# Optimization experiments

Measured on AMD Instinct MI355X. Metric: run time of the kernel, lower is better.

Reference implementation:

```python
import jax, jax.numpy as jnp
import numpy as np

B, T, F, H = 64, 512, 128, 512

def _rnn(x_seq, h0, Wih, Whh, bih, bhh):
    # PyTorch vanilla RNN: h_t = tanh(x_t @ Wih^T + bih + h_{t-1} @ Whh^T + bhh)
    def step(h, x_t):
        h = jnp.tanh(x_t @ Wih.T + bih + h @ Whh.T + bhh)
        return h, h
    _, ys = jax.lax.scan(step, h0, jnp.swapaxes(x_seq, 0, 1))  # scan over time
    return jnp.swapaxes(ys, 0, 1)  # [B, T, H]

def _decode(z, Wih, Whh, bih, bhh):
    # decoder input at step t = concat(prev_output, z_t); 1-layer RNN so prev_output == h_{t-1}
    def step(h, z_t):
        u = jnp.concatenate([h, z_t], axis=-1)  # [B, 2H]
        h_new = jnp.tanh(u @ Wih.T + bih + h @ Whh.T + bhh)
        return h_new, h_new
    h0 = jnp.zeros((z.shape[0], Whh.shape[0]), z.dtype)
    _, ys = jax.lax.scan(step, h0, jnp.swapaxes(z, 0, 1))
    return jnp.swapaxes(ys, 0, 1)  # [B, T, H]

def setup_inputs() -> dict:
    key = jax.random.key(0)
    ks = jax.random.split(key, 16)
    s = 0.02
    p = {
        'x':   jax.random.normal(ks[0], (B, T, F), jnp.float32),
        'eps': jax.random.normal(ks[1], (B, T, H), jnp.float32),
        'Wih_en': jax.random.normal(ks[2], (H, F)) * s,
        'Whh_en': jax.random.normal(ks[3], (H, H)) * s,
        'bih_en': jax.random.normal(ks[4], (H,)) * s,
        'bhh_en': jax.random.normal(ks[5], (H,)) * s,
        'W_mu':  jax.random.normal(ks[6], (H, H)) * s,
        'b_mu':  jax.random.normal(ks[7], (H,)) * s,
        'W_lv':  jax.random.normal(ks[8], (H, H)) * s,
        'b_lv':  jax.random.normal(ks[9], (H,)) * s,
        'Wih_de': jax.random.normal(ks[10], (H, 2 * H)) * s,
        'Whh_de': jax.random.normal(ks[11], (H, H)) * s,
        'bih_de': jax.random.normal(ks[12], (H,)) * s,
        'bhh_de': jax.random.normal(ks[13], (H,)) * s,
        'W_mux': jax.random.normal(ks[14], (F, H)) * s,
        'b_mux': jnp.zeros((F,)),
        'W_lvx': jax.random.normal(ks[15], (F, H)) * s,
        'b_lvx': jnp.zeros((F,)),
    }
    return p

def reference(x, eps, Wih_en, Whh_en, bih_en, bhh_en, W_mu, b_mu, W_lv, b_lv,
              Wih_de, Whh_de, bih_de, bhh_de, W_mux, b_mux, W_lvx, b_lvx):
    h0 = jnp.zeros((x.shape[0], Whh_en.shape[0]), x.dtype)
    y = _rnn(x, h0, Wih_en, Whh_en, bih_en, bhh_en)                 # [B,T,H]
    mu_post = y @ W_mu.T + b_mu
    logsigma2_post = y @ W_lv.T + b_lv
    z = eps * jnp.exp(logsigma2_post / 2) + mu_post                 # reparameterize
    outputs = _decode(z, Wih_de, Whh_de, bih_de, bhh_de)            # [B,T,H]
    mu_xhat = outputs @ W_mux.T + b_mux
    logsigma2_xhat = outputs @ W_lvx.T + b_lvx
    return (mu_post, logsigma2_post, mu_xhat, logsigma2_xhat)
```

## Files before the change

kernel.cpp:

```cpp
#include <hip/hip_runtime.h>

typedef _Float16 h2_t __attribute__((ext_vector_type(2)));
typedef _Float16 h4_t __attribute__((ext_vector_type(4)));
typedef _Float16 h8_t __attribute__((ext_vector_type(8)));
typedef float    f4_t __attribute__((ext_vector_type(4)));

#define B_  64
#define T_  512
#define F_  128
#define H_  512

static __device__ __forceinline__ float fdot2f(h2_t a, h2_t b, float c) {
#if __has_builtin(__builtin_amdgcn_fdot2)
    return __builtin_amdgcn_fdot2(a, b, c, false);
#else
    return c + (float)a.x * (float)b.x + (float)a.y * (float)b.y;
#endif
}

static __device__ __forceinline__ void dot8(float& acc, uint4 w, uint4 h) {
    acc = fdot2f(__builtin_bit_cast(h2_t, w.x), __builtin_bit_cast(h2_t, h.x), acc);
    acc = fdot2f(__builtin_bit_cast(h2_t, w.y), __builtin_bit_cast(h2_t, h.y), acc);
    acc = fdot2f(__builtin_bit_cast(h2_t, w.z), __builtin_bit_cast(h2_t, h.z), acc);
    acc = fdot2f(__builtin_bit_cast(h2_t, w.w), __builtin_bit_cast(h2_t, h.w), acc);
}

static __device__ __forceinline__ int d4(int acc, unsigned a, unsigned b) {
#if __has_builtin(__builtin_amdgcn_sdot4)
    return __builtin_amdgcn_sdot4((int)a, (int)b, acc, false);
#else
    #pragma unroll
    for (int i = 0; i < 4; ++i)
        acc += (int)(signed char)((a >> (8 * i)) & 0xff) *
               (int)(signed char)((b >> (8 * i)) & 0xff);
    return acc;
#endif
}
static __device__ __forceinline__ int dot16i8(int acc, uint4 w, uint4 h) {
    acc = d4(acc, w.x, h.x);
    acc = d4(acc, w.y, h.y);
    acc = d4(acc, w.z, h.z);
    acc = d4(acc, w.w, h.w);
    return acc;
}

__global__ void k_cast_f16(const float* __restrict__ src, _Float16* __restrict__ dst, int n) {
    int i = blockIdx.x * blockDim.x + threadIdx.x;
    if (i < n) dst[i] = (_Float16)src[i];
}

__global__ void k_prep_z(const float* __restrict__ Wih_de, _Float16* __restrict__ Wz) {
    int i = blockIdx.x * blockDim.x + threadIdx.x;
    int cc = i >> 9, kk = i & 511;
    Wz[i] = (_Float16)Wih_de[cc * 1024 + 512 + kk];
}

__global__ void k_prep_bias(const float* __restrict__ a, const float* __restrict__ b,
                            float* __restrict__ o) {
    int i = threadIdx.x;
    o[i] = a[i] + b[i];
}

__global__ void k_quant(const float* __restrict__ A, int sA,
                        const float* __restrict__ Bo, int sB,
                        signed char* __restrict__ q, float* __restrict__ fac) {
    __shared__ float red[128];
    const int c = blockIdx.x, t = threadIdx.x;
    f4_t v = *(const f4_t*)(A + (size_t)c * sA + t * 4);
    if (Bo) {
        f4_t vb = *(const f4_t*)(Bo + (size_t)c * sB + t * 4);
        v = v + vb;
    }
    float m = fmaxf(fmaxf(fabsf(v[0]), fabsf(v[1])), fmaxf(fabsf(v[2]), fabsf(v[3])));
    red[t] = m;
    __syncthreads();
    for (int o = 64; o; o >>= 1) {
        if (t < o) red[t] = fmaxf(red[t], red[t + o]);
        __syncthreads();
    }
    float mx = red[0];
    float inv = mx > 0.f ? 127.f / mx : 0.f;
    unsigned r = 0;
    #pragma unroll
    for (int i = 0; i < 4; ++i) {
        int qi = (int)rintf(fminf(fmaxf(v[i] * inv, -127.f), 127.f));
        r |= ((unsigned)(unsigned char)(signed char)qi) << (8 * i);
    }
    *(unsigned*)(q + (size_t)c * 512 + t * 4) = r;
    if (t == 0) fac[c] = mx > 0.f ? mx / 127.f : 0.f;
}

#define BM 128
#define BN 128
#define BK 32
#define LDT 40

__global__ __launch_bounds__(256) void k_gemm(
    const _Float16* __restrict__ A, const _Float16* __restrict__ Bt,
    const float* __restrict__ bias,
    float* __restrict__ Cf, _Float16* __restrict__ Ch,
    int M, int N, int K) {
    __shared__ _Float16 Al[BM * LDT];
    __shared__ _Float16 Bl[BN * LDT];
    const int tid = threadIdx.x;
    const int bm = blockIdx.x * BM, bn = blockIdx.y * BN;
    const int wid = tid >> 6, lane = tid & 63;
    const int wm = (wid >> 1) * 64, wn = (wid & 1) * 64;
    const int l15 = lane & 15, l4 = lane >> 4;

    f4_t acc[4][4];
    #pragma unroll
    for (int i = 0; i < 4; ++i)
        #pragma unroll
        for (int j = 0; j < 4; ++j) {
            f4_t zz = {0.f, 0.f, 0.f, 0.f};
            acc[i][j] = zz;
        }

    const int r = tid >> 1, hf = tid & 1;
    const h8_t* gA0 = (const h8_t*)(A + (size_t)(bm + r) * K);
    const h8_t* gB0 = (const h8_t*)(Bt + (size_t)(bn + r) * K);

    for (int k0 = 0; k0 < K; k0 += BK) {
        __syncthreads();
        int kf = (k0 >> 3) + hf * 2;
        h8_t a0 = gA0[kf], a1 = gA0[kf + 1];
        h8_t b0 = gB0[kf], b1 = gB0[kf + 1];
        *(h8_t*)&Al[r * LDT + hf * 16]     = a0;
        *(h8_t*)&Al[r * LDT + hf * 16 + 8] = a1;
        *(h8_t*)&Bl[r * LDT + hf * 16]     = b0;
        *(h8_t*)&Bl[r * LDT + hf * 16 + 8] = b1;
        __syncthreads();
        h8_t af[4], bf[4];
        #pragma unroll
        for (int i = 0; i < 4; ++i) af[i] = *(const h8_t*)&Al[(wm + i * 16 + l15) * LDT + l4 * 8];
        #pragma unroll
        for (int j = 0; j < 4; ++j) bf[j] = *(const h8_t*)&Bl[(wn + j * 16 + l15) * LDT + l4 * 8];
        #pragma unroll
        for (int i = 0; i < 4; ++i)
            #pragma unroll
            for (int j = 0; j < 4; ++j)
                acc[i][j] = __builtin_amdgcn_mfma_f32_16x16x32_f16(af[i], bf[j], acc[i][j], 0, 0, 0);
    }

    #pragma unroll
    for (int i = 0; i < 4; ++i) {
        int m0 = bm + wm + i * 16 + l4 * 4;
        #pragma unroll
        for (int j = 0; j < 4; ++j) {
            int n0 = bn + wn + j * 16 + l15;
            float bb = bias ? bias[n0] : 0.f;
            #pragma unroll
            for (int rr = 0; rr < 4; ++rr) {
                float v = acc[i][j][rr] + bb;
                size_t off = (size_t)(m0 + rr) * N + n0;
                if (Cf) Cf[off] = v;
                if (Ch) Ch[off] = (_Float16)v;
            }
        }
    }
}

__global__ __launch_bounds__(512) void k_rnn(
    const signed char* __restrict__ Wq,
    const float* __restrict__ fac,
    const _Float16* __restrict__ pre,
    _Float16* __restrict__ out) {
    __shared__ __align__(16) signed char h_q[H_];
    __shared__ int ipart[H_];

    const int tid = threadIdx.x;
    const int c2 = tid & 255;
    const int s = tid >> 8;
    const int b = blockIdx.x;

    const uint4* q0 = (const uint4*)(Wq + (size_t)c2 * 512 + s * 256);
    const uint4* q1 = (const uint4*)(Wq + (size_t)(c2 + 256) * 512 + s * 256);
    uint4 wa[16], wb[16];
    #pragma unroll
    for (int j = 0; j < 16; ++j) { wa[j] = q0[j]; wb[j] = q1[j]; }
    if (tid < 32) ((uint4*)h_q)[tid] = make_uint4(0u, 0u, 0u, 0u);
    __syncthreads();

    const size_t base = (size_t)b * T_ * H_ + tid;
    float pcur = (float)pre[base];
    const float facr = fac[tid] * (1.f / 127.f);

    for (int t = 0; t < T_; ++t) {
        int tn = (t + 1 < T_) ? t + 1 : t;
        _Float16 pnx = pre[base + (size_t)tn * H_];

        int i0 = 0, i1 = 0;
        const uint4* hv = ((const uint4*)h_q) + s * 16;
        #pragma unroll
        for (int j = 0; j < 16; ++j) {
            uint4 hh = hv[j];
            i0 = dot16i8(i0, wa[j], hh);
            i1 = dot16i8(i1, wb[j], hh);
        }

        ipart[tid ^ 256] = s ? i0 : i1;
        __syncthreads();
        int mine = s ? i1 : i0;
        float hn = tanhf((float)(mine + ipart[tid]) * facr + pcur);
        out[base + (size_t)t * H_] = (_Float16)hn;
        h_q[tid] = (signed char)(int)rintf(hn * 127.f);
        __syncthreads();
        pcur = (float)pnx;
    }
}

__global__ void k_z(const float* __restrict__ mu, const float* __restrict__ lv,
                    const float* __restrict__ eps, _Float16* __restrict__ z, int n4) {
    int i = blockIdx.x * blockDim.x + threadIdx.x;
    if (i >= n4) return;
    f4_t m = ((const f4_t*)mu)[i];
    f4_t l = ((const f4_t*)lv)[i];
    f4_t e = ((const f4_t*)eps)[i];
    h4_t r;
    #pragma unroll
    for (int j = 0; j < 4; ++j) r[j] = (_Float16)(e[j] * expf(l[j] * 0.5f) + m[j]);
    ((h4_t*)z)[i] = r;
}

extern "C" void kernel_launch(void* const* d_in, const int* in_sizes, int n_in,
                              void* d_out, int out_size, void* d_ws, size_t ws_size,
                              hipStream_t stream) {
    const float* x      = (const float*)d_in[0];
    const float* eps    = (const float*)d_in[1];
    const float* Wih_en = (const float*)d_in[2];
    const float* Whh_en = (const float*)d_in[3];
    const float* bih_en = (const float*)d_in[4];
    const float* bhh_en = (const float*)d_in[5];
    const float* W_mu   = (const float*)d_in[6];
    const float* b_mu   = (const float*)d_in[7];
    const float* W_lv   = (const float*)d_in[8];
    const float* b_lv   = (const float*)d_in[9];
    const float* Wih_de = (const float*)d_in[10];
    const float* Whh_de = (const float*)d_in[11];
    const float* bih_de = (const float*)d_in[12];
    const float* bhh_de = (const float*)d_in[13];
    const float* W_mux  = (const float*)d_in[14];
    const float* b_mux  = (const float*)d_in[15];
    const float* W_lvx  = (const float*)d_in[16];
    const float* b_lvx  = (const float*)d_in[17];
    float* out = (float*)d_out;

    char* ws = (char*)d_ws;
    _Float16* Wih_en_h = (_Float16*)(ws + 0);
    _Float16* W_mu_h   = (_Float16*)(ws + 655360);
    _Float16* W_lv_h   = (_Float16*)(ws + 1179648);
    _Float16* Wz_h     = (_Float16*)(ws + 1703936);
    _Float16* Wmux_h   = (_Float16*)(ws + 2752512);
    _Float16* Wlvx_h   = (_Float16*)(ws + 2883584);
    float*    benc     = (float*)(ws + 3014656);
    float*    bdec     = (float*)(ws + 3016704);
    signed char* Wq_en = (signed char*)(ws + 3018752);
    signed char* Wq_de = (signed char*)(ws + 3280896);
    float*    fac_en   = (float*)(ws + 3543040);
    float*    fac_de   = (float*)(ws + 3545088);
    _Float16* x_h      = (_Float16*)(ws + 4194304);
    _Float16* pre_h    = (_Float16*)(ws + 12582912);
    _Float16* act_h    = (_Float16*)(ws + 46137344);
    _Float16* z_h      = (_Float16*)(ws + 79691776);

    const int thr = 256;
    k_cast_f16<<<(65536 + thr - 1) / thr, thr, 0, stream>>>(Wih_en, Wih_en_h, 65536);
    k_cast_f16<<<(262144 + thr - 1) / thr, thr, 0, stream>>>(W_mu, W_mu_h, 262144);
    k_cast_f16<<<(262144 + thr - 1) / thr, thr, 0, stream>>>(W_lv, W_lv_h, 262144);
    k_cast_f16<<<(65536 + thr - 1) / thr, thr, 0, stream>>>(W_mux, Wmux_h, 65536);
    k_cast_f16<<<(65536 + thr - 1) / thr, thr, 0, stream>>>(W_lvx, Wlvx_h, 65536);
    k_cast_f16<<<(4194304 + thr - 1) / thr, thr, 0, stream>>>(x, x_h, 4194304);
    k_prep_z<<<262144 / thr, thr, 0, stream>>>(Wih_de, Wz_h);
    k_prep_bias<<<1, 512, 0, stream>>>(bih_en, bhh_en, benc);
    k_prep_bias<<<1, 512, 0, stream>>>(bih_de, bhh_de, bdec);
    k_quant<<<512, 128, 0, stream>>>(Whh_en, 512, nullptr, 0, Wq_en, fac_en);
    k_quant<<<512, 128, 0, stream>>>(Wih_de, 1024, Whh_de, 512, Wq_de, fac_de);

    dim3 gFull(32768 / BM, 512 / BN);
    dim3 gNarrow(32768 / BM, 1);

    k_gemm<<<gFull, 256, 0, stream>>>(x_h, Wih_en_h, benc, nullptr, pre_h, 32768, 512, 128);
    k_rnn<<<64, 512, 0, stream>>>(Wq_en, fac_en, pre_h, act_h);
    k_gemm<<<gFull, 256, 0, stream>>>(act_h, W_mu_h, b_mu, out, nullptr, 32768, 512, 512);
    k_gemm<<<gFull, 256, 0, stream>>>(act_h, W_lv_h, b_lv, out + 16777216, nullptr, 32768, 512, 512);
    k_z<<<4194304 / thr, thr, 0, stream>>>(out, out + 16777216, eps, z_h, 4194304);
    k_gemm<<<gFull, 256, 0, stream>>>(z_h, Wz_h, bdec, nullptr, pre_h, 32768, 512, 512);
    k_rnn<<<64, 512, 0, stream>>>(Wq_de, fac_de, pre_h, act_h);
    k_gemm<<<gNarrow, 256, 0, stream>>>(act_h, Wmux_h, b_mux, out + 33554432, nullptr, 32768, 128, 512);
    k_gemm<<<gNarrow, 256, 0, stream>>>(act_h, Wlvx_h, b_lvx, out + 37748736, nullptr, 32768, 128, 512);
}
```

Before: 1.108 ms.

## Split RNN dot products across lane quads with DPP reduction and double-buffered state

Reorganizes the int8 recurrent kernel so each group of four lanes computes four hidden rows, each lane covering a 128-wide K slice, and partial sums are combined with DPP quad reductions instead of a shared-memory exchange. The hidden-state buffer is double-buffered with padded rows, which removes one of the two block barriers per timestep. Part of the weight slice is spilled to LDS to fit register limits, adding LDS reads each step and extra shuffle work.

```diff
diff --git a/kernel.cpp b/kernel.cpp
--- a/kernel.cpp
+++ b/kernel.cpp
@@ -42,6 +42,17 @@
     acc = d4(acc, w.z, h.z);
     acc = d4(acc, w.w, h.w);
     return acc;
+}
+
+static __device__ __forceinline__ int quad_sum(int x) {
+#if __has_builtin(__builtin_amdgcn_mov_dpp)
+    x += __builtin_amdgcn_mov_dpp(x, 0xB1, 0xF, 0xF, true);
+    x += __builtin_amdgcn_mov_dpp(x, 0x4E, 0xF, 0xF, true);
+#else
+    x += __shfl_xor(x, 1);
+    x += __shfl_xor(x, 2);
+#endif
+    return x;
 }
 
 __global__ void k_cast_f16(const float* __restrict__ src, _Float16* __restrict__ dst, int n) {
@@ -161,50 +172,78 @@
     }
 }
 
+#define HQS 144
 __global__ __launch_bounds__(512) void k_rnn(
     const signed char* __restrict__ Wq,
     const float* __restrict__ fac,
     const _Float16* __restrict__ pre,
     _Float16* __restrict__ out) {
-    __shared__ __align__(16) signed char h_q[H_];
-    __shared__ int ipart[H_];
+    __shared__ __align__(16) signed char h_q[2][4 * HQS];
+    __shared__ __align__(16) uint4 WL[2 * 512];
 
     const int tid = threadIdx.x;
-    const int c2 = tid & 255;
-    const int s = tid >> 8;
+    const int q = tid & 3;
+    const int g = tid >> 2;
+    const int row = 4 * g + q;
     const int b = blockIdx.x;
 
-    const uint4* q0 = (const uint4*)(Wq + (size_t)c2 * 512 + s * 256);
-    const uint4* q1 = (const uint4*)(Wq + (size_t)(c2 + 256) * 512 + s * 256);
-    uint4 wa[16], wb[16];
-    #pragma unroll
-    for (int j = 0; j < 16; ++j) { wa[j] = q0[j]; wb[j] = q1[j]; }
-    if (tid < 32) ((uint4*)h_q)[tid] = make_uint4(0u, 0u, 0u, 0u);
+    const uint4* g0 = (const uint4*)(Wq + (size_t)(4 * g + 0) * 512 + q * 128);
+    const uint4* g1 = (const uint4*)(Wq + (size_t)(4 * g + 1) * 512 + q * 128);
+    const uint4* g2 = (const uint4*)(Wq + (size_t)(4 * g + 2) * 512 + q * 128);
+    const uint4* g3 = (const uint4*)(Wq + (size_t)(4 * g + 3) * 512 + q * 128);
+    uint4 w0[8], w1[8], w2[8], w3[6];
+    #pragma unroll
+    for (int j = 0; j < 8; ++j) { w0[j] = g0[j]; w1[j] = g1[j]; w2[j] = g2[j]; }
+    #pragma unroll
+    for (int j = 0; j < 6; ++j) w3[j] = g3[j];
+    WL[tid]       = g3[6];
+    WL[512 + tid] = g3[7];
+    if (tid < 36) ((uint4*)&h_q[0][0])[tid] = make_uint4(0u, 0u, 0u, 0u);
     __syncthreads();
 
-    const size_t base = (size_t)b * T_ * H_ + tid;
+    const size_t base = (size_t)b * T_ * H_ + row;
     float pcur = (float)pre[base];
-    const float facr = fac[tid] * (1.f / 127.f);
+    const float facr = fac[row] * (1.f / 127.f);
+    const int hwoff = ((row >> 7) * HQS) + (row & 127);
 
     for (int t = 0; t < T_; ++t) {
         int tn = (t + 1 < T_) ? t + 1 : t;
         _Float16 pnx = pre[base + (size_t)tn * H_];
 
-        int i0 = 0, i1 = 0;
-        const uint4* hv = ((const uint4*)h_q) + s * 16;
-        #pragma unroll
-        for (int j = 0; j < 16; ++j) {
+        const uint4* hv = (const uint4*)&h_q[t & 1][q * HQS];
+        int a0 = 0, a1 = 0, a2 = 0, a3 = 0;
+        #pragma unroll
+        for (int j = 0; j < 6; ++j) {
             uint4 hh = hv[j];
-            i0 = dot16i8(i0, wa[j], hh);
-            i1 = dot16i8(i1, wb[j], hh);
-        }
-
-        ipart[tid ^ 256] = s ? i0 : i1;
-        __syncthreads();
-        int mine = s ? i1 : i0;
-        float hn = tanhf((float)(mine + ipart[tid]) * facr + pcur);
+            a0 = dot16i8(a0, w0[j], hh);
+            a1 = dot16i8(a1, w1[j], hh);
+            a2 = dot16i8(a2, w2[j], hh);
+            a3 = dot16i8(a3, w3[j], hh);
+        }
+        {
+            uint4 hh = hv[6];
+            a0 = dot16i8(a0, w0[6], hh);
+            a1 = dot16i8(a1, w1[6], hh);
+            a2 = dot16i8(a2, w2[6], hh);
+            a3 = dot16i8(a3, WL[tid], hh);
+        }
+        {
+            uint4 hh = hv[7];
+            a0 = dot16i8(a0, w0[7], hh);
+            a1 = dot16i8(a1, w1[7], hh);
+            a2 = dot16i8(a2, w2[7], hh);
+            a3 = dot16i8(a3, WL[512 + tid], hh);
+        }
+
+        a0 = quad_sum(a0);
+        a1 = quad_sum(a1);
+        a2 = quad_sum(a2);
+        a3 = quad_sum(a3);
+        int mine = (q == 0) ? a0 : (q == 1) ? a1 : (q == 2) ? a2 : a3;
+
+        float hn = tanhf((float)mine * facr + pcur);
         out[base + (size_t)t * H_] = (_Float16)hn;
-        h_q[tid] = (signed char)(int)rintf(hn * 127.f);
+        h_q[(t + 1) & 1][hwoff] = (signed char)(int)rintf(hn * 127.f);
         __syncthreads();
         pcur = (float)pnx;
     }
```

New measurement: 1.142 ms. 3.0% more time.

## Pair-split RNN rows with DPP reduction and fuse twin output GEMMs

Applied to the files above, without the earlier changes.

The recurrent kernel now maps each adjacent thread pair to two hidden rows, with each thread covering one half of the K dimension. The partial sums are combined with a DPP lane swap instead of a shared-memory exchange, and the hidden-state buffer is double-buffered. This removes one block-wide barrier and one LDS round trip from every timestep of the serial recurrence. Separately, the mu/logvar and mux/lvx projection pairs are each computed by a single wider GEMM launch that splits its output columns into two destinations. This relies on the paired fp16 weight buffers sitting next to each other in the workspace, and concatenated bias vectors are built for it.

```diff
diff --git a/kernel.cpp b/kernel.cpp
--- a/kernel.cpp
+++ b/kernel.cpp
@@ -9,21 +9,6 @@
 #define T_  512
 #define F_  128
 #define H_  512
-
-static __device__ __forceinline__ float fdot2f(h2_t a, h2_t b, float c) {
-#if __has_builtin(__builtin_amdgcn_fdot2)
-    return __builtin_amdgcn_fdot2(a, b, c, false);
-#else
-    return c + (float)a.x * (float)b.x + (float)a.y * (float)b.y;
-#endif
-}
-
-static __device__ __forceinline__ void dot8(float& acc, uint4 w, uint4 h) {
-    acc = fdot2f(__builtin_bit_cast(h2_t, w.x), __builtin_bit_cast(h2_t, h.x), acc);
-    acc = fdot2f(__builtin_bit_cast(h2_t, w.y), __builtin_bit_cast(h2_t, h.y), acc);
-    acc = fdot2f(__builtin_bit_cast(h2_t, w.z), __builtin_bit_cast(h2_t, h.z), acc);
-    acc = fdot2f(__builtin_bit_cast(h2_t, w.w), __builtin_bit_cast(h2_t, h.w), acc);
-}
 
 static __device__ __forceinline__ int d4(int acc, unsigned a, unsigned b) {
 #if __has_builtin(__builtin_amdgcn_sdot4)
@@ -44,6 +29,14 @@
     return acc;
 }
 
+static __device__ __forceinline__ int pair_sum(int x) {
+#if __has_builtin(__builtin_amdgcn_mov_dpp)
+    return x + __builtin_amdgcn_mov_dpp(x, 0xB1, 0xF, 0xF, true);
+#else
+    return x + __shfl_xor(x, 1);
+#endif
+}
+
 __global__ void k_cast_f16(const float* __restrict__ src, _Float16* __restrict__ dst, int n) {
     int i = blockIdx.x * blockDim.x + threadIdx.x;
     if (i < n) dst[i] = (_Float16)src[i];
@@ -59,6 +52,12 @@
                             float* __restrict__ o) {
     int i = threadIdx.x;
     o[i] = a[i] + b[i];
+}
+
+__global__ void k_cat2(const float* __restrict__ a, const float* __restrict__ b,
+                       float* __restrict__ o, int n) {
+    int i = blockIdx.x * blockDim.x + threadIdx.x;
+    if (i < 2 * n) o[i] = (i < n) ? a[i] : b[i - n];
 }
 
 __global__ void k_quant(const float* __restrict__ A, int sA,
@@ -98,8 +97,8 @@
 __global__ __launch_bounds__(256) void k_gemm(
     const _Float16* __restrict__ A, const _Float16* __restrict__ Bt,
     const float* __restrict__ bias,
-    float* __restrict__ Cf, _Float16* __restrict__ Ch,
-    int M, int N, int K) {
+    float* __restrict__ Cf, float* __restrict__ Cf2, _Float16* __restrict__ Ch,
+    int M, int N, int nsplit, int K) {
     __shared__ _Float16 Al[BM * LDT];
     __shared__ _Float16 Bl[BN * LDT];
     const int tid = threadIdx.x;
@@ -143,6 +142,7 @@
                 acc[i][j] = __builtin_amdgcn_mfma_f32_16x16x32_f16(af[i], bf[j], acc[i][j], 0, 0, 0);
     }
 
+    const int ns2 = N - nsplit;
     #pragma unroll
     for (int i = 0; i < 4; ++i) {
         int m0 = bm + wm + i * 16 + l4 * 4;
@@ -153,9 +153,11 @@
             #pragma unroll
             for (int rr = 0; rr < 4; ++rr) {
                 float v = acc[i][j][rr] + bb;
-                size_t off = (size_t)(m0 + rr) * N + n0;
-                if (Cf) Cf[off] = v;
-                if (Ch) Ch[off] = (_Float16)v;
+                if (Cf) {
+                    if (n0 < nsplit) Cf[(size_t)(m0 + rr) * nsplit + n0] = v;
+                    else             Cf2[(size_t)(m0 + rr) * ns2 + (n0 - nsplit)] = v;
+                }
+                if (Ch) Ch[(size_t)(m0 + rr) * N + n0] = (_Float16)v;
             }
         }
     }
@@ -166,20 +168,20 @@
     const float* __restrict__ fac,
     const _Float16* __restrict__ pre,
     _Float16* __restrict__ out) {
-    __shared__ __align__(16) signed char h_q[H_];
-    __shared__ int ipart[H_];
+    __shared__ __align__(16) signed char h_q[2][H_];
 
     const int tid = threadIdx.x;
-    const int c2 = tid & 255;
-    const int s = tid >> 8;
+    const int half = tid & 1;
+    const int r0 = tid & ~1;
+    const int r1 = tid | 1;
     const int b = blockIdx.x;
 
-    const uint4* q0 = (const uint4*)(Wq + (size_t)c2 * 512 + s * 256);
-    const uint4* q1 = (const uint4*)(Wq + (size_t)(c2 + 256) * 512 + s * 256);
+    const uint4* q0 = (const uint4*)(Wq + (size_t)r0 * 512 + half * 256);
+    const uint4* q1 = (const uint4*)(Wq + (size_t)r1 * 512 + half * 256);
     uint4 wa[16], wb[16];
     #pragma unroll
     for (int j = 0; j < 16; ++j) { wa[j] = q0[j]; wb[j] = q1[j]; }
-    if (tid < 32) ((uint4*)h_q)[tid] = make_uint4(0u, 0u, 0u, 0u);
+    if (tid < 32) ((uint4*)&h_q[0][0])[tid] = make_uint4(0u, 0u, 0u, 0u);
     __syncthreads();
 
     const size_t base = (size_t)b * T_ * H_ + tid;
@@ -191,7 +193,7 @@
         _Float16 pnx = pre[base + (size_t)tn * H_];
 
         int i0 = 0, i1 = 0;
-        const uint4* hv = ((const uint4*)h_q) + s * 16;
+        const uint4* hv = ((const uint4*)&h_q[t & 1][0]) + half * 16;
         #pragma unroll
         for (int j = 0; j < 16; ++j) {
             uint4 hh = hv[j];
@@ -199,12 +201,13 @@
             i1 = dot16i8(i1, wb[j], hh);
         }
 
-        ipart[tid ^ 256] = s ? i0 : i1;
-        __syncthreads();
-        int mine = s ? i1 : i0;
-        float hn = tanhf((float)(mine + ipart[tid]) * facr + pcur);
+        int o0 = pair_sum(i0);
+        int o1 = pair_sum(i1);
+        int mine = half ? o1 : o0;
+
+        float hn = tanhf((float)mine * facr + pcur);
         out[base + (size_t)t * H_] = (_Float16)hn;
-        h_q[tid] = (signed char)(int)rintf(hn * 127.f);
+        h_q[(t + 1) & 1][tid] = (signed char)(int)rintf(hn * 127.f);
         __syncthreads();
         pcur = (float)pnx;
     }
@@ -259,6 +262,8 @@
     signed char* Wq_de = (signed char*)(ws + 3280896);
     float*    fac_en   = (float*)(ws + 3543040);
     float*    fac_de   = (float*)(ws + 3545088);
+    float*    bmulv    = (float*)(ws + 3547136);
+    float*    bmuxlvx  = (float*)(ws + 3551232);
     _Float16* x_h      = (_Float16*)(ws + 4194304);
     _Float16* pre_h    = (_Float16*)(ws + 12582912);
     _Float16* act_h    = (_Float16*)(ws + 46137344);
@@ -274,19 +279,24 @@
     k_prep_z<<<262144 / thr, thr, 0, stream>>>(Wih_de, Wz_h);
     k_prep_bias<<<1, 512, 0, stream>>>(bih_en, bhh_en, benc);
     k_prep_bias<<<1, 512, 0, stream>>>(bih_de, bhh_de, bdec);
+    k_cat2<<<4, 256, 0, stream>>>(b_mu, b_lv, bmulv, 512);
+    k_cat2<<<1, 256, 0, stream>>>(b_mux, b_lvx, bmuxlvx, 128);
     k_quant<<<512, 128, 0, stream>>>(Whh_en, 512, nullptr, 0, Wq_en, fac_en);
     k_quant<<<512, 128, 0, stream>>>(Wih_de, 1024, Whh_de, 512, Wq_de, fac_de);
 
     dim3 gFull(32768 / BM, 512 / BN);
-    dim3 gNarrow(32768 / BM, 1);
-
-    k_gemm<<<gFull, 256, 0, stream>>>(x_h, Wih_en_h, benc, nullptr, pre_h, 32768, 512, 128);
+    dim3 gWide(32768 / BM, 1024 / BN);
+    dim3 gNarrow(32768 / BM, 256 / BN);
+
+    k_gemm<<<gFull, 256, 0, stream>>>(x_h, Wih_en_h, benc, nullptr, nullptr, pre_h,
+                                      32768, 512, 512, 128);
     k_rnn<<<64, 512, 0, stream>>>(Wq_en, fac_en, pre_h, act_h);
-    k_gemm<<<gFull, 256, 0, stream>>>(act_h, W_mu_h, b_mu, out, nullptr, 32768, 512, 512);
-    k_gemm<<<gFull, 256, 0, stream>>>(act_h, W_lv_h, b_lv, out + 16777216, nullptr, 32768, 512, 512);
+    k_gemm<<<gWide, 256, 0, stream>>>(act_h, W_mu_h, bmulv, out, out + 16777216, nullptr,
+                                      32768, 1024, 512, 512);
     k_z<<<4194304 / thr, thr, 0, stream>>>(out, out + 16777216, eps, z_h, 4194304);
-    k_gemm<<<gFull, 256, 0, stream>>>(z_h, Wz_h, bdec, nullptr, pre_h, 32768, 512, 512);
+    k_gemm<<<gFull, 256, 0, stream>>>(z_h, Wz_h, bdec, nullptr, nullptr, pre_h,
+                                      32768, 512, 512, 512);
     k_rnn<<<64, 512, 0, stream>>>(Wq_de, fac_de, pre_h, act_h);
-    k_gemm<<<gNarrow, 256, 0, stream>>>(act_h, Wmux_h, b_mux, out + 33554432, nullptr, 32768, 128, 512);
-    k_gemm<<<gNarrow, 256, 0, stream>>>(act_h, Wlvx_h, b_lvx, out + 37748736, nullptr, 32768, 128, 512);
-}
+    k_gemm<<<gNarrow, 256, 0, stream>>>(act_h, Wmux_h, bmuxlvx, out + 33554432, out + 37748736,
+                                        nullptr, 32768, 256, 128, 512);
+}
```

Result: faster. 1.069 ms (-3.6%).
